# Kernel optimization log

Measured on AMD Instinct MI355X. Metric: run time of the kernel, lower is better.

The kernel has to match this reference:

```python
import jax, jax.numpy as jnp
import numpy as np

B, C, E, H = 8, 2048, 1024, 128


def setup_inputs() -> dict:
    key = jax.random.key(0)
    kx, kq, kk, kv = jax.random.split(key, 4)
    scale = 1.0 / np.sqrt(E)
    return {
        "x": jax.random.normal(kx, (B, C, E), dtype=jnp.float32),
        "Wq": jax.random.normal(kq, (E, H), dtype=jnp.float32) * scale,
        "Wk": jax.random.normal(kk, (E, H), dtype=jnp.float32) * scale,
        "Wv": jax.random.normal(kv, (E, H), dtype=jnp.float32) * scale,
    }


def reference(x, Wq, Wk, Wv):
    # x: (B, C, E); projections -> (B, C, H)
    q = jnp.einsum("bce,eh->bch", x, Wq)
    k = jnp.einsum("bce,eh->bch", x, Wk)
    v = jnp.einsum("bce,eh->bch", x, Wv)
    # NOTE: original scales by sqrt(embed_size), not head_size
    scores = jnp.einsum("bqh,bkh->bqk", q, k) / jnp.sqrt(jnp.asarray(E, x.dtype))
    Cq = x.shape[1]
    causal = jnp.tril(jnp.ones((Cq, Cq), dtype=bool))
    scores = jnp.where(causal, scores, -jnp.inf)
    weights = jax.nn.softmax(scores, axis=-1)  # (B, C, C)
    out = jnp.einsum("bqk,bkh->bqh", weights, v)
    return out
```

## Files before the change

### kernel.cpp

```cpp
#include <hip/hip_runtime.h>
#include <hip/hip_bf16.h>

#define BATCH 8
#define CTX   2048
#define EMB   1024
#define HD    128
#define VSTR  2080

using bf16x8 = __attribute__((ext_vector_type(8))) short;
using fx4    = __attribute__((ext_vector_type(4))) float;

__device__ __forceinline__ ushort f2bf(float f) {
    union { float f; unsigned u; } v; v.f = f;
    unsigned u = v.u;
    u += 0x7fffu + ((u >> 16) & 1u);
    return (ushort)(u >> 16);
}

__device__ __forceinline__ unsigned cvtpk(float a, float b) {
    unsigned r;
    asm("v_cvt_pk_bf16_f32 %0, %1, %2" : "=v"(r) : "v"(a), "v"(b));
    return r;
}

__device__ __forceinline__ float exp2a(float x) {
    float r;
    asm("v_exp_f32 %0, %1" : "=v"(r) : "v"(x));
    return r;
}

__device__ __forceinline__ void gload16(const void* g, void* l) {
    __builtin_amdgcn_global_load_lds(
        (const __attribute__((address_space(1))) unsigned*)g,
        (__attribute__((address_space(3))) unsigned*)l, 16, 0, 0);
}

__global__ void wt_kernel(const float* __restrict__ Wq, const float* __restrict__ Wk,
                          const float* __restrict__ Wv, ushort* __restrict__ Wt) {
    int idx = blockIdx.x * blockDim.x + threadIdx.x;
    int e = idx % EMB;
    int h = (idx / EMB) % HD;
    int w = idx / (EMB * HD);
    const float* W = (w == 0) ? Wq : (w == 1) ? Wk : Wv;
    Wt[idx] = f2bf(W[e * HD + h]);
}

__global__ __launch_bounds__(256) void proj_kernel(
        const float* __restrict__ x, const ushort* __restrict__ Wt,
        ushort* __restrict__ q, ushort* __restrict__ k, ushort* __restrict__ vt) {
    __shared__ __align__(16) float  As[32 * 64];
    __shared__ __align__(16) ushort Bs[192 * 64];

    const int t    = threadIdx.x;
    const int wave = t >> 6;
    const int lane = t & 63;
    const int lo = lane & 15, hi = lane >> 4;
    const int brow = blockIdx.x * 32;
    const int bcol = blockIdx.y * 192;

    const char* Ab = (const char*)As;
    const char* Bb = (const char*)Bs;

    fx4 acc[2][3];
#pragma unroll
    for (int m2 = 0; m2 < 2; m2++)
#pragma unroll
        for (int n = 0; n < 3; n++) acc[m2][n] = fx4{0.f, 0.f, 0.f, 0.f};

    const int arow_s = t >> 4;
    const int acol_s = ((t & 15) ^ (arow_s & 7)) << 2;
    const int brow_s = t >> 3;
    const int bcol_s = ((t & 7) ^ (brow_s & 7)) << 3;
    const int ldsbase = wave * 1024;

    for (int k0 = 0; k0 < EMB; k0 += 64) {
#pragma unroll
        for (int r = 0; r < 2; r++)
            gload16(x + (size_t)(brow + r * 16 + arow_s) * EMB + k0 + acol_s,
                    (char*)As + r * 4096 + ldsbase);
#pragma unroll
        for (int r = 0; r < 6; r++)
            gload16(Wt + (size_t)(bcol + r * 32 + brow_s) * EMB + k0 + bcol_s,
                    (char*)Bs + r * 4096 + ldsbase);
        __syncthreads();

#pragma unroll
        for (int ks = 0; ks < 2; ks++) {
            bf16x8 af[2], bfr[3];
#pragma unroll
            for (int m2 = 0; m2 < 2; m2++) {
                const int rowA = m2 * 16 + lo;
                const unsigned sw = (rowA & 7) << 4;
                const unsigned ub = rowA * 256 + ks * 128 + hi * 32;
                fx4 a0 = *(const fx4*)(Ab + (ub ^ sw));
                fx4 a1 = *(const fx4*)(Ab + ((ub + 16) ^ sw));
                union { unsigned u[4]; bf16x8 v; } pk;
                pk.u[0] = cvtpk(a0[0], a0[1]);
                pk.u[1] = cvtpk(a0[2], a0[3]);
                pk.u[2] = cvtpk(a1[0], a1[1]);
                pk.u[3] = cvtpk(a1[2], a1[3]);
                af[m2] = pk.v;
            }
#pragma unroll
            for (int n = 0; n < 3; n++) {
                const int rowB = wave * 48 + n * 16 + lo;
                const unsigned ub = rowB * 128 + ks * 64 + hi * 16;
                bfr[n] = *(const bf16x8*)(Bb + (ub ^ ((rowB & 7) << 4)));
            }
#pragma unroll
            for (int m2 = 0; m2 < 2; m2++)
#pragma unroll
                for (int n = 0; n < 3; n++)
                    acc[m2][n] = __builtin_amdgcn_mfma_f32_16x16x32_bf16(af[m2], bfr[n], acc[m2][n], 0, 0, 0);
        }
        __syncthreads();
    }

    const float qscale = 0.045084219f;
#pragma unroll
    for (int n = 0; n < 3; n++) {
        const int col = bcol + wave * 48 + n * 16 + lo;
        const int bnn = col >> 7;
        const int cc  = col & 127;
#pragma unroll
        for (int m2 = 0; m2 < 2; m2++) {
#pragma unroll
            for (int j = 0; j < 4; j++) {
                const int r = brow + m2 * 16 + hi * 4 + j;
                if (bnn == 0)      q[(size_t)r * HD + cc] = f2bf(acc[m2][n][j] * qscale);
                else if (bnn == 1) k[(size_t)r * HD + cc] = f2bf(acc[m2][n][j]);
                else {
                    const int bb2 = r >> 11, ccc = r & (CTX - 1);
                    vt[((size_t)bb2 * HD + cc) * VSTR + ccc] = f2bf(acc[m2][n][j]);
                }
            }
        }
    }
}

__global__ __launch_bounds__(128) void attn_kernel(
        const ushort* __restrict__ q, const ushort* __restrict__ k,
        const ushort* __restrict__ vt, float* __restrict__ out) {
    __shared__ __align__(16) char Ks[2][2][8192];
    __shared__ __align__(16) char p_lds[2][1280];

    const int id   = blockIdx.x;
    const int b    = id & 7;
    const int pos  = id >> 3;
    const int qt   = (pos < 64) ? (127 - pos) : (pos - 64);
    const int q0   = qt * 16;
    const int t    = threadIdx.x;
    const int w    = t >> 6;
    const int lane = t & 63;
    const int lo = lane & 15, hi = lane >> 4;

    const ushort* qb = q  + (size_t)b * CTX * HD;
    const ushort* kb = k  + (size_t)b * CTX * HD;
    const ushort* vb = vt + (size_t)b * HD * VSTR;

    bf16x8 qf[4];
#pragma unroll
    for (int ks = 0; ks < 4; ks++)
        qf[ks] = *(const bf16x8*)(qb + (q0 + lo) * HD + ks * 32 + hi * 8);

    fx4 o[8];
#pragma unroll
    for (int h = 0; h < 8; h++) o[h] = fx4{0.f, 0.f, 0.f, 0.f};
    float m[4], l[4];
#pragma unroll
    for (int j = 0; j < 4; j++) { m[j] = 0.f; l[j] = 0.f; }

#define KSTAGE(bi, kv0_) do {                                                  \
    _Pragma("unroll")                                                          \
    for (int r = 0; r < 8; ++r) {                                              \
        const int rl  = r * 4 + (lane >> 4);                                   \
        const int key = (rl >> 1) & 7;                                         \
        gload16(kb + (size_t)((kv0_) + w * 32 + rl) * HD + (((lane & 15) ^ key) << 3), \
                Ks[bi][w] + r * 1024);                                         \
    }                                                                          \
} while (0)

    const int nkv = qt / 4 + 1;
    KSTAGE(0, 0);

    for (int it = 0; it < nkv; ++it) {
        const int kv0 = it * 64;
        bf16x8 vf[8];
#pragma unroll
        for (int h = 0; h < 8; h++)
            vf[h] = *(const bf16x8*)(vb + (size_t)(h * 16 + lo) * VSTR + kv0 + w * 32 + hi * 8);
        __builtin_amdgcn_sched_barrier(0);
        if (it + 1 < nkv) {
            KSTAGE((it + 1) & 1, kv0 + 64);
            __builtin_amdgcn_sched_barrier(0);
            asm volatile("s_waitcnt vmcnt(16)" ::: "memory");
        } else {
            asm volatile("s_waitcnt vmcnt(8)" ::: "memory");
        }
        __builtin_amdgcn_sched_barrier(0);

        const char* Kb = Ks[it & 1][w];
        fx4 s[2];
        s[0] = fx4{0.f, 0.f, 0.f, 0.f};
        s[1] = fx4{0.f, 0.f, 0.f, 0.f};
        __builtin_amdgcn_s_setprio(1);
#pragma unroll
        for (int n2 = 0; n2 < 2; n2++) {
            const int rl = 2 * lo + n2;
#pragma unroll
            for (int ks = 0; ks < 4; ks++) {
                bf16x8 kf = *(const bf16x8*)(Kb + rl * 256 + ((ks * 64 + hi * 16) ^ ((lo & 7) << 4)));
                s[n2] = __builtin_amdgcn_mfma_f32_16x16x32_bf16(qf[ks], kf, s[n2], 0, 0, 0);
            }
        }
        __builtin_amdgcn_s_setprio(0);

        const bool diag = (kv0 + 64 > q0);
        float pmax[4];
        int allok = 1;
#pragma unroll
        for (int j = 0; j < 4; j++) {
            const int r = q0 + hi * 4 + j;
            if (diag) {
                const int c0 = kv0 + w * 32 + 2 * lo;
                if (c0 > r)     s[0][j] = -INFINITY;
                if (c0 + 1 > r) s[1][j] = -INFINITY;
            }
            pmax[j] = fmaxf(s[0][j], s[1][j]);
            allok &= (pmax[j] <= m[j] + 23.0f);
        }
        if (!__all(allok)) {
#pragma unroll
            for (int j = 0; j < 4; j++) {
                float mx = pmax[j];
                mx = fmaxf(mx, __shfl_xor(mx, 1));
                mx = fmaxf(mx, __shfl_xor(mx, 2));
                mx = fmaxf(mx, __shfl_xor(mx, 4));
                mx = fmaxf(mx, __shfl_xor(mx, 8));
                const float mn = fmaxf(m[j], mx);
                const float f  = exp2a(m[j] - mn);
                l[j] *= f;
#pragma unroll
                for (int h = 0; h < 8; h++) o[h][j] *= f;
                m[j] = mn;
            }
        }
#pragma unroll
        for (int j = 0; j < 4; j++) {
            const float p0 = exp2a(s[0][j] - m[j]);
            const float p1 = exp2a(s[1][j] - m[j]);
            l[j] += p0 + p1;
            *(unsigned*)(p_lds[w] + (hi * 4 + j) * 80 + lo * 4) = cvtpk(p0, p1);
        }
        asm volatile("" ::: "memory");
        bf16x8 pa = *(const bf16x8*)(p_lds[w] + lo * 80 + hi * 16);
        __builtin_amdgcn_s_setprio(1);
#pragma unroll
        for (int h = 0; h < 8; h++)
            o[h] = __builtin_amdgcn_mfma_f32_16x16x32_bf16(pa, vf[h], o[h], 0, 0, 0);
        __builtin_amdgcn_s_setprio(0);
    }
#undef KSTAGE

#pragma unroll
    for (int j = 0; j < 4; j++) {
        l[j] += __shfl_xor(l[j], 1);
        l[j] += __shfl_xor(l[j], 2);
        l[j] += __shfl_xor(l[j], 4);
        l[j] += __shfl_xor(l[j], 8);
    }

    float* oB  = (float*)&Ks[0][0][0];
    float* mlB = (float*)&Ks[1][0][0];
    __syncthreads();
    if (w == 1) {
#pragma unroll
        for (int j = 0; j < 4; j++) {
            const int row = hi * 4 + j;
            if (lo == 0) { mlB[row] = m[j]; mlB[16 + row] = l[j]; }
#pragma unroll
            for (int h = 0; h < 8; h++) oB[row * 128 + h * 16 + lo] = o[h][j];
        }
    }
    __syncthreads();
    if (w == 0) {
        float* ob = out + ((size_t)b * CTX + q0) * HD;
#pragma unroll
        for (int j = 0; j < 4; j++) {
            const int row = hi * 4 + j;
            const float mB = mlB[row], lB = mlB[16 + row];
            const float mt = fmaxf(m[j], mB);
            const float fA = exp2a(m[j] - mt);
            const float fB = exp2a(mB - mt);
            const float inv = 1.0f / (l[j] * fA + lB * fB);
#pragma unroll
            for (int h = 0; h < 8; h++)
                ob[row * HD + h * 16 + lo] =
                    (o[h][j] * fA + oB[row * 128 + h * 16 + lo] * fB) * inv;
        }
    }
}

extern "C" void kernel_launch(void* const* d_in, const int* in_sizes, int n_in,
                              void* d_out, int out_size, void* d_ws, size_t ws_size,
                              hipStream_t stream) {
    const float* x  = (const float*)d_in[0];
    const float* Wq = (const float*)d_in[1];
    const float* Wk = (const float*)d_in[2];
    const float* Wv = (const float*)d_in[3];

    ushort* Wt = (ushort*)d_ws;
    ushort* qw = (ushort*)((char*)d_ws + 786432);
    ushort* kw = qw + (size_t)BATCH * CTX * HD;
    ushort* vw = kw + (size_t)BATCH * CTX * HD;

    wt_kernel<<<(3 * HD * EMB) / 256, 256, 0, stream>>>(Wq, Wk, Wv, Wt);
    proj_kernel<<<dim3(512, 2), 256, 0, stream>>>(x, Wt, qw, kw, vw);
    attn_kernel<<<1024, 128, 0, stream>>>(qw, kw, vw, (float*)d_out);
}
```

Before: 85.77 us.

## Pair causal query tiles per block and split KV across four waves

The attention kernel now runs 512 blocks of 256 threads. Each block processes two query tiles in sequence, one long (127-p) and one short (p), which balances causal work across blocks. Four waves each take a 32-key slice of a 128-key step, and the partial softmax states from all four are merged through LDS. Separately, the projection kernel rotates the starting K-chunk per block so that concurrent blocks spread their reads across the reduction dimension. The costs are extra LDS traffic and syncthreads for the four-way merge, a larger LDS footprint per block, and fewer resident blocks.

```diff
diff --git a/kernel.cpp b/kernel.cpp
--- a/kernel.cpp
+++ b/kernel.cpp
@@ -57,6 +57,7 @@
     const int lo = lane & 15, hi = lane >> 4;
     const int brow = blockIdx.x * 32;
     const int bcol = blockIdx.y * 192;
+    const int kph  = (blockIdx.x ^ (blockIdx.y << 3)) & 15;
 
     const char* Ab = (const char*)As;
     const char* Bb = (const char*)Bs;
@@ -73,7 +74,8 @@
     const int bcol_s = ((t & 7) ^ (brow_s & 7)) << 3;
     const int ldsbase = wave * 1024;
 
-    for (int k0 = 0; k0 < EMB; k0 += 64) {
+    for (int i = 0; i < 16; ++i) {
+        const int k0 = ((i + kph) & 15) << 6;
 #pragma unroll
         for (int r = 0; r < 2; r++)
             gload16(x + (size_t)(brow + r * 16 + arow_s) * EMB + k0 + acol_s,
@@ -138,17 +140,15 @@
     }
 }
 
-__global__ __launch_bounds__(128) void attn_kernel(
+__global__ __launch_bounds__(256) void attn_kernel(
         const ushort* __restrict__ q, const ushort* __restrict__ k,
         const ushort* __restrict__ vt, float* __restrict__ out) {
-    __shared__ __align__(16) char Ks[2][2][8192];
-    __shared__ __align__(16) char p_lds[2][1280];
+    __shared__ __align__(16) char Ks[2][4][8192];
+    __shared__ __align__(16) char p_lds[4][1280];
 
     const int id   = blockIdx.x;
     const int b    = id & 7;
-    const int pos  = id >> 3;
-    const int qt   = (pos < 64) ? (127 - pos) : (pos - 64);
-    const int q0   = qt * 16;
+    const int p    = id >> 3;
     const int t    = threadIdx.x;
     const int w    = t >> 6;
     const int lane = t & 63;
@@ -158,17 +158,8 @@
     const ushort* kb = k  + (size_t)b * CTX * HD;
     const ushort* vb = vt + (size_t)b * HD * VSTR;
 
-    bf16x8 qf[4];
-#pragma unroll
-    for (int ks = 0; ks < 4; ks++)
-        qf[ks] = *(const bf16x8*)(qb + (q0 + lo) * HD + ks * 32 + hi * 8);
-
-    fx4 o[8];
-#pragma unroll
-    for (int h = 0; h < 8; h++) o[h] = fx4{0.f, 0.f, 0.f, 0.f};
-    float m[4], l[4];
-#pragma unroll
-    for (int j = 0; j < 4; j++) { m[j] = 0.f; l[j] = 0.f; }
+    float* oB  = (float*)&Ks[0][0][0];
+    float* mlB = (float*)&Ks[0][3][0];
 
 #define KSTAGE(bi, kv0_) do {                                                  \
     _Pragma("unroll")                                                          \
@@ -180,125 +171,155 @@
     }                                                                          \
 } while (0)
 
-    const int nkv = qt / 4 + 1;
-    KSTAGE(0, 0);
-
-    for (int it = 0; it < nkv; ++it) {
-        const int kv0 = it * 64;
-        bf16x8 vf[8];
-#pragma unroll
-        for (int h = 0; h < 8; h++)
-            vf[h] = *(const bf16x8*)(vb + (size_t)(h * 16 + lo) * VSTR + kv0 + w * 32 + hi * 8);
-        __builtin_amdgcn_sched_barrier(0);
-        if (it + 1 < nkv) {
-            KSTAGE((it + 1) & 1, kv0 + 64);
+    for (int phase = 0; phase < 2; ++phase) {
+        const int qt = phase ? p : (127 - p);
+        const int q0 = qt * 16;
+        const int nkv = qt / 8 + 1;
+
+        bf16x8 qf[4];
+#pragma unroll
+        for (int ks = 0; ks < 4; ks++)
+            qf[ks] = *(const bf16x8*)(qb + (q0 + lo) * HD + ks * 32 + hi * 8);
+
+        fx4 o[8];
+#pragma unroll
+        for (int h = 0; h < 8; h++) o[h] = fx4{0.f, 0.f, 0.f, 0.f};
+        float m[4], l[4];
+#pragma unroll
+        for (int j = 0; j < 4; j++) { m[j] = 0.f; l[j] = 0.f; }
+
+        KSTAGE(0, 0);
+
+        for (int it = 0; it < nkv; ++it) {
+            const int kv0 = it * 128;
+            bf16x8 vf[8];
+#pragma unroll
+            for (int h = 0; h < 8; h++)
+                vf[h] = *(const bf16x8*)(vb + (size_t)(h * 16 + lo) * VSTR + kv0 + w * 32 + hi * 8);
             __builtin_amdgcn_sched_barrier(0);
-            asm volatile("s_waitcnt vmcnt(16)" ::: "memory");
-        } else {
-            asm volatile("s_waitcnt vmcnt(8)" ::: "memory");
-        }
-        __builtin_amdgcn_sched_barrier(0);
-
-        const char* Kb = Ks[it & 1][w];
-        fx4 s[2];
-        s[0] = fx4{0.f, 0.f, 0.f, 0.f};
-        s[1] = fx4{0.f, 0.f, 0.f, 0.f};
-        __builtin_amdgcn_s_setprio(1);
-#pragma unroll
-        for (int n2 = 0; n2 < 2; n2++) {
-            const int rl = 2 * lo + n2;
-#pragma unroll
-            for (int ks = 0; ks < 4; ks++) {
-                bf16x8 kf = *(const bf16x8*)(Kb + rl * 256 + ((ks * 64 + hi * 16) ^ ((lo & 7) << 4)));
-                s[n2] = __builtin_amdgcn_mfma_f32_16x16x32_bf16(qf[ks], kf, s[n2], 0, 0, 0);
-            }
-        }
-        __builtin_amdgcn_s_setprio(0);
-
-        const bool diag = (kv0 + 64 > q0);
-        float pmax[4];
-        int allok = 1;
+            if (it + 1 < nkv) {
+                KSTAGE((it + 1) & 1, kv0 + 128);
+                __builtin_amdgcn_sched_barrier(0);
+                asm volatile("s_waitcnt vmcnt(16)" ::: "memory");
+            } else {
+                asm volatile("s_waitcnt vmcnt(8)" ::: "memory");
+            }
+            __builtin_amdgcn_sched_barrier(0);
+
+            const char* Kb = Ks[it & 1][w];
+            fx4 s[2];
+            s[0] = fx4{0.f, 0.f, 0.f, 0.f};
+            s[1] = fx4{0.f, 0.f, 0.f, 0.f};
+            __builtin_amdgcn_s_setprio(1);
+#pragma unroll
+            for (int n2 = 0; n2 < 2; n2++) {
+                const int rl = 2 * lo + n2;
+#pragma unroll
+                for (int ks = 0; ks < 4; ks++) {
+                    bf16x8 kf = *(const bf16x8*)(Kb + rl * 256 + ((ks * 64 + hi * 16) ^ ((lo & 7) << 4)));
+                    s[n2] = __builtin_amdgcn_mfma_f32_16x16x32_bf16(qf[ks], kf, s[n2], 0, 0, 0);
+                }
+            }
+            __builtin_amdgcn_s_setprio(0);
+
+            const bool diag = (kv0 + 128 > q0);
+            float pmax[4];
+            int allok = 1;
+#pragma unroll
+            for (int j = 0; j < 4; j++) {
+                const int r = q0 + hi * 4 + j;
+                if (diag) {
+                    const int c0 = kv0 + w * 32 + 2 * lo;
+                    if (c0 > r)     s[0][j] = -INFINITY;
+                    if (c0 + 1 > r) s[1][j] = -INFINITY;
+                }
+                pmax[j] = fmaxf(s[0][j], s[1][j]);
+                allok &= (pmax[j] <= m[j] + 23.0f);
+            }
+            if (!__all(allok)) {
+#pragma unroll
+                for (int j = 0; j < 4; j++) {
+                    float mx = pmax[j];
+                    mx = fmaxf(mx, __shfl_xor(mx, 1));
+                    mx = fmaxf(mx, __shfl_xor(mx, 2));
+                    mx = fmaxf(mx, __shfl_xor(mx, 4));
+                    mx = fmaxf(mx, __shfl_xor(mx, 8));
+                    const float mn = fmaxf(m[j], mx);
+                    const float f  = exp2a(m[j] - mn);
+                    l[j] *= f;
+#pragma unroll
+                    for (int h = 0; h < 8; h++) o[h][j] *= f;
+                    m[j] = mn;
+                }
+            }
+#pragma unroll
+            for (int j = 0; j < 4; j++) {
+                const float p0 = exp2a(s[0][j] - m[j]);
+                const float p1 = exp2a(s[1][j] - m[j]);
+                l[j] += p0 + p1;
+                *(unsigned*)(p_lds[w] + (hi * 4 + j) * 80 + lo * 4) = cvtpk(p0, p1);
+            }
+            asm volatile("" ::: "memory");
+            bf16x8 pa = *(const bf16x8*)(p_lds[w] + lo * 80 + hi * 16);
+            __builtin_amdgcn_s_setprio(1);
+#pragma unroll
+            for (int h = 0; h < 8; h++)
+                o[h] = __builtin_amdgcn_mfma_f32_16x16x32_bf16(pa, vf[h], o[h], 0, 0, 0);
+            __builtin_amdgcn_s_setprio(0);
+        }
+
 #pragma unroll
         for (int j = 0; j < 4; j++) {
-            const int r = q0 + hi * 4 + j;
-            if (diag) {
-                const int c0 = kv0 + w * 32 + 2 * lo;
-                if (c0 > r)     s[0][j] = -INFINITY;
-                if (c0 + 1 > r) s[1][j] = -INFINITY;
-            }
-            pmax[j] = fmaxf(s[0][j], s[1][j]);
-            allok &= (pmax[j] <= m[j] + 23.0f);
-        }
-        if (!__all(allok)) {
-#pragma unroll
-            for (int j = 0; j < 4; j++) {
-                float mx = pmax[j];
-                mx = fmaxf(mx, __shfl_xor(mx, 1));
-                mx = fmaxf(mx, __shfl_xor(mx, 2));
-                mx = fmaxf(mx, __shfl_xor(mx, 4));
-                mx = fmaxf(mx, __shfl_xor(mx, 8));
-                const float mn = fmaxf(m[j], mx);
-                const float f  = exp2a(m[j] - mn);
-                l[j] *= f;
-#pragma unroll
-                for (int h = 0; h < 8; h++) o[h][j] *= f;
-                m[j] = mn;
-            }
-        }
-#pragma unroll
-        for (int j = 0; j < 4; j++) {
-            const float p0 = exp2a(s[0][j] - m[j]);
-            const float p1 = exp2a(s[1][j] - m[j]);
-            l[j] += p0 + p1;
-            *(unsigned*)(p_lds[w] + (hi * 4 + j) * 80 + lo * 4) = cvtpk(p0, p1);
-        }
-        asm volatile("" ::: "memory");
-        bf16x8 pa = *(const bf16x8*)(p_lds[w] + lo * 80 + hi * 16);
-        __builtin_amdgcn_s_setprio(1);
-#pragma unroll
-        for (int h = 0; h < 8; h++)
-            o[h] = __builtin_amdgcn_mfma_f32_16x16x32_bf16(pa, vf[h], o[h], 0, 0, 0);
-        __builtin_amdgcn_s_setprio(0);
+            l[j] += __shfl_xor(l[j], 1);
+            l[j] += __shfl_xor(l[j], 2);
+            l[j] += __shfl_xor(l[j], 4);
+            l[j] += __shfl_xor(l[j], 8);
+        }
+
+        __syncthreads();
+        if (w > 0) {
+#pragma unroll
+            for (int j = 0; j < 4; j++) {
+                const int row = hi * 4 + j;
+                if (lo == 0) { mlB[(w - 1) * 32 + row] = m[j]; mlB[(w - 1) * 32 + 16 + row] = l[j]; }
+#pragma unroll
+                for (int h = 0; h < 8; h++)
+                    oB[(w - 1) * 2048 + row * 128 + h * 16 + lo] = o[h][j];
+            }
+        }
+        __syncthreads();
+        if (w == 0) {
+            float* ob = out + ((size_t)b * CTX + q0) * HD;
+#pragma unroll
+            for (int j = 0; j < 4; j++) {
+                const int row = hi * 4 + j;
+                float mp[3], lp[3];
+                float mt = m[j];
+#pragma unroll
+                for (int pp = 0; pp < 3; pp++) {
+                    mp[pp] = mlB[pp * 32 + row];
+                    lp[pp] = mlB[pp * 32 + 16 + row];
+                    mt = fmaxf(mt, mp[pp]);
+                }
+                const float f0 = exp2a(m[j] - mt);
+                float fp[3];
+#pragma unroll
+                for (int pp = 0; pp < 3; pp++) fp[pp] = exp2a(mp[pp] - mt);
+                const float inv = 1.0f / (l[j] * f0 + lp[0] * fp[0] + lp[1] * fp[1] + lp[2] * fp[2]);
+#pragma unroll
+                for (int h = 0; h < 8; h++) {
+                    float acc = o[h][j] * f0;
+#pragma unroll
+                    for (int pp = 0; pp < 3; pp++)
+                        acc += oB[pp * 2048 + row * 128 + h * 16 + lo] * fp[pp];
+                    ob[row * HD + h * 16 + lo] = acc * inv;
+                }
+            }
+        }
+        __syncthreads();
+        asm volatile("s_waitcnt vmcnt(0)" ::: "memory");
     }
 #undef KSTAGE
-
-#pragma unroll
-    for (int j = 0; j < 4; j++) {
-        l[j] += __shfl_xor(l[j], 1);
-        l[j] += __shfl_xor(l[j], 2);
-        l[j] += __shfl_xor(l[j], 4);
-        l[j] += __shfl_xor(l[j], 8);
-    }
-
-    float* oB  = (float*)&Ks[0][0][0];
-    float* mlB = (float*)&Ks[1][0][0];
-    __syncthreads();
-    if (w == 1) {
-#pragma unroll
-        for (int j = 0; j < 4; j++) {
-            const int row = hi * 4 + j;
-            if (lo == 0) { mlB[row] = m[j]; mlB[16 + row] = l[j]; }
-#pragma unroll
-            for (int h = 0; h < 8; h++) oB[row * 128 + h * 16 + lo] = o[h][j];
-        }
-    }
-    __syncthreads();
-    if (w == 0) {
-        float* ob = out + ((size_t)b * CTX + q0) * HD;
-#pragma unroll
-        for (int j = 0; j < 4; j++) {
-            const int row = hi * 4 + j;
-            const float mB = mlB[row], lB = mlB[16 + row];
-            const float mt = fmaxf(m[j], mB);
-            const float fA = exp2a(m[j] - mt);
-            const float fB = exp2a(mB - mt);
-            const float inv = 1.0f / (l[j] * fA + lB * fB);
-#pragma unroll
-            for (int h = 0; h < 8; h++)
-                ob[row * HD + h * 16 + lo] =
-                    (o[h][j] * fA + oB[row * 128 + h * 16 + lo] * fB) * inv;
-        }
-    }
 }
 
 extern "C" void kernel_launch(void* const* d_in, const int* in_sizes, int n_in,
@@ -316,5 +337,5 @@
 
     wt_kernel<<<(3 * HD * EMB) / 256, 256, 0, stream>>>(Wq, Wk, Wv, Wt);
     proj_kernel<<<dim3(512, 2), 256, 0, stream>>>(x, Wt, qw, kw, vw);
-    attn_kernel<<<1024, 128, 0, stream>>>(qw, kw, vw, (float*)d_out);
-}
+    attn_kernel<<<512, 256, 0, stream>>>(qw, kw, vw, (float*)d_out);
+}
```

New measurement: 84.83 us. Within noise of the previous version (-1.1%).
